# Optimization experiments

Hardware: AMD Instinct MI355X
Metric: run time of the kernel (lower is better)

## Reference

```python
import jax, jax.numpy as jnp
import numpy as np

PILLAR_GROUPS = [[0,1,2],[3,4],[5,6],[7,8,9],[10,11],[12,13,14],[15,16],[17,18],[19],[20,21,22],[23,24,25],[26,27,28]]
N_GROUPS = len(PILLAR_GROUPS)      # 12
MAX_G = max(len(g) for g in PILLAR_GROUPS)  # 3
ENC_DIM = 8
EPS = 1e-5

# static padded gather indices + validity mask so all 12 encoders run in one einsum
_idx = np.zeros((N_GROUPS, MAX_G), np.int32)
_msk = np.zeros((N_GROUPS, MAX_G), np.float32)
for _i, _g in enumerate(PILLAR_GROUPS):
    _idx[_i, :len(_g)] = _g
    _msk[_i, :len(_g)] = 1.0
IDX = jnp.asarray(_idx)
MASK = jnp.asarray(_msk)


def bn(h, gamma, beta, mean, var):
    # BatchNorm1d in eval mode (running statistics)
    return gamma * (h - mean) * jax.lax.rsqrt(var + EPS) + beta


def setup_inputs() -> dict:
    key = jax.random.key(0)
    ks = jax.random.split(key, 40)
    B = 524288

    def rn(k, shape, s=0.2):
        return jax.random.normal(k, shape, jnp.float32) * s

    def bn_params(k, d):
        k1, k2, k3, k4 = jax.random.split(k, 4)
        return (1.0 + rn(k1, (d,), 0.05),          # gamma
                rn(k2, (d,), 0.05),                 # beta
                rn(k3, (d,), 0.1),                  # running_mean
                0.5 + jax.random.uniform(k4, (d,), jnp.float32))  # running_var > 0

    g1, bb1, m1, v1 = bn_params(ks[10], 64)
    g2, bb2, m2, v2 = bn_params(ks[11], 32)
    g3, bb3, m3, v3 = bn_params(ks[12], 16)
    eg, ebt, em, ev = bn_params(ks[13], ENC_DIM)
    # per-encoder BN params: [12, 8]
    eg = jnp.tile(eg, (N_GROUPS, 1)) + rn(ks[14], (N_GROUPS, ENC_DIM), 0.02)
    ebt = jnp.tile(ebt, (N_GROUPS, 1)) + rn(ks[15], (N_GROUPS, ENC_DIM), 0.02)
    em = jnp.tile(em, (N_GROUPS, 1)) + rn(ks[16], (N_GROUPS, ENC_DIM), 0.02)
    ev = jnp.tile(ev, (N_GROUPS, 1)) + 0.1 * jax.random.uniform(ks[17], (N_GROUPS, ENC_DIM))

    return {
        "x": jax.random.normal(ks[0], (B, 29), jnp.float32),
        "We": rn(ks[1], (N_GROUPS, MAX_G, ENC_DIM)),  # padded; pad rows hit zeroed x
        "be": rn(ks[2], (N_GROUPS, ENC_DIM)),
        "enc_gamma": eg, "enc_beta": ebt, "enc_mean": em, "enc_var": ev,
        "Wa": rn(ks[3], (ENC_DIM * N_GROUPS, N_GROUPS)),
        "ba": rn(ks[4], (N_GROUPS,)),
        "W1": rn(ks[5], (ENC_DIM * N_GROUPS, 64)), "b1": rn(ks[6], (64,)),
        "g1": g1, "bb1": bb1, "m1": m1, "v1": v1,
        "W2": rn(ks[7], (64, 32)), "b2": rn(ks[8], (32,)),
        "g2": g2, "bb2": bb2, "m2": m2, "v2": v2,
        "W3": rn(ks[9], (32, 16)), "b3": rn(ks[18], (16,)),
        "g3": g3, "bb3": bb3, "m3": m3, "v3": v3,
        "W4": rn(ks[19], (16, 1)), "b4": rn(ks[20], (1,)),
    }


def reference(x, We, be, enc_gamma, enc_beta, enc_mean, enc_var,
              Wa, ba, W1, b1, g1, bb1, m1, v1,
              W2, b2, g2, bb2, m2, v2,
              W3, b3, g3, bb3, m3, v3, W4, b4):
    B = x.shape[0]
    # gather each pillar group (padded to MAX_G, pads zeroed) -> [B, 12, 3]
    xg = x[:, IDX] * MASK
    # all 12 encoders: Linear + ReLU + BN(eval)  -> reps [B, 12, 8]
    reps = jax.nn.relu(jnp.einsum('bgi,gio->bgo', xg, We) + be)
    reps = bn(reps, enc_gamma, enc_beta, enc_mean, enc_var)
    stacked = reps.reshape(B, -1)                      # [B, 96] (cat order matches)
    weights = jax.nn.softmax(stacked @ Wa + ba, axis=1)  # [B, 12]
    attended = (reps * weights[:, :, None]).reshape(B, -1)  # [B, 96]
    h = bn(jax.nn.relu(attended @ W1 + b1), g1, bb1, m1, v1)  # dropout = identity (eval)
    h = bn(jax.nn.relu(h @ W2 + b2), g2, bb2, m2, v2)
    h = bn(jax.nn.relu(h @ W3 + b3), g3, bb3, m3, v3)
    return jax.nn.sigmoid(h @ W4 + b4)[:, 0]           # squeeze(1) -> [B]
```

## Files before the change

### kernel.cpp

```cpp
#include <hip/hip_runtime.h>
#include <math.h>


typedef _Float16 f16x8 __attribute__((ext_vector_type(8)));
typedef float    f32x4 __attribute__((ext_vector_type(4)));

#define EPS 1e-5f

__device__ __forceinline__ float rcp_fast(float v) { return __builtin_amdgcn_rcpf(v); }

__host__ __device__ constexpr unsigned long long packGS() {
    constexpr int gs[12] = {0,3,5,7,10,12,15,17,19,20,23,26};
    unsigned long long v = 0;
    for (int g = 0; g < 12; ++g) v |= (unsigned long long)gs[g] << (5*g);
    return v;
}
__host__ __device__ constexpr unsigned packGL() {
    constexpr int gl[12] = {3,2,2,3,2,3,2,2,1,3,3,3};
    unsigned v = 0;
    for (int g = 0; g < 12; ++g) v |= (unsigned)gl[g] << (2*g);
    return v;
}

__global__ __launch_bounds__(256, 2) void fused_kernel(
    const float* __restrict__ x,
    const float* __restrict__ We,  const float* __restrict__ be,
    const float* __restrict__ eg,  const float* __restrict__ ebt,
    const float* __restrict__ em,  const float* __restrict__ ev,
    const float* __restrict__ Wa,  const float* __restrict__ ba,
    const float* __restrict__ W1,  const float* __restrict__ b1,
    const float* __restrict__ g1,  const float* __restrict__ bb1,
    const float* __restrict__ m1,  const float* __restrict__ v1,
    const float* __restrict__ W2,  const float* __restrict__ b2,
    const float* __restrict__ g2,  const float* __restrict__ bb2,
    const float* __restrict__ m2,  const float* __restrict__ v2,
    const float* __restrict__ W3,  const float* __restrict__ b3,
    const float* __restrict__ g3,  const float* __restrict__ bb3,
    const float* __restrict__ m3,  const float* __restrict__ v3,
    const float* __restrict__ W4,  const float* __restrict__ b4,
    float* __restrict__ out, int B, int ntiles)
{
    __shared__ __align__(16) char smem_raw[32768];
    const int lane = threadIdx.x & 63;
    const int wave = threadIdx.x >> 6;
    const int l15  = lane & 15;
    const int quad = lane >> 4;

    char* sw = smem_raw + wave * 8192;
    _Float16* repT = (_Float16*)(sw);
    float*    wT   = (float*)   (sw + 3328);
    _Float16* h1T  = (_Float16*)(sw + 4416);
    _Float16* h2T  = (_Float16*)(sw + 6720);

    constexpr unsigned long long GS = packGS();
    constexpr unsigned GL = packGL();

    f16x8 Benc[6];
    #pragma unroll
    for (int t = 0; t < 6; ++t) {
        const int n = t*16 + l15;
        const int g = n >> 3, o = n & 7;
        const int gs = (int)((GS >> (5*g)) & 31);
        const int gl = (int)((GL >> (2*g)) & 3);
        #pragma unroll
        for (int j = 0; j < 8; ++j) {
            const int k  = quad*8 + j;
            const int ji = k - gs;
            float v = (ji >= 0 && ji < gl) ? We[(g*3 + ji)*8 + o] : 0.f;
            Benc[t][j] = (_Float16)v;
        }
    }
    f16x8 Bwa[3];
    #pragma unroll
    for (int s = 0; s < 3; ++s) {
        #pragma unroll
        for (int j = 0; j < 8; ++j) {
            const int k = s*32 + quad*8 + j;
            float v = (l15 < 12) ? Wa[k*12 + l15] : 0.f;
            Bwa[s][j] = (_Float16)v;
        }
    }
    f16x8 Bw1[12];
    #pragma unroll
    for (int t = 0; t < 4; ++t)
        #pragma unroll
        for (int s = 0; s < 3; ++s)
            #pragma unroll
            for (int j = 0; j < 8; ++j) {
                const int k = s*32 + quad*8 + j;
                Bw1[t*3 + s][j] = (_Float16)W1[k*64 + t*16 + l15];
            }
    f16x8 Bw2[4];
    #pragma unroll
    for (int t = 0; t < 2; ++t)
        #pragma unroll
        for (int s = 0; s < 2; ++s)
            #pragma unroll
            for (int j = 0; j < 8; ++j) {
                const int k = s*32 + quad*8 + j;
                Bw2[t*2 + s][j] = (_Float16)W2[k*32 + t*16 + l15];
            }
    f16x8 Bw3;
    #pragma unroll
    for (int j = 0; j < 8; ++j)
        Bw3[j] = (_Float16)W3[(quad*8 + j)*16 + l15];

    float encB[6], encS[6], encT[6];
    #pragma unroll
    for (int t = 0; t < 6; ++t) {
        const int c = t*16 + l15;
        float s = eg[c] * rsqrtf(ev[c] + EPS);
        encS[t] = s; encT[t] = ebt[c] - em[c]*s; encB[t] = be[c];
    }
    const float baL = (l15 < 12) ? ba[l15] : -1e4f;
    float b1L[4], s1L[4], t1L[4];
    #pragma unroll
    for (int t = 0; t < 4; ++t) {
        const int c = t*16 + l15;
        float s = g1[c] * rsqrtf(v1[c] + EPS);
        s1L[t] = s; t1L[t] = bb1[c] - m1[c]*s; b1L[t] = b1[c];
    }
    float b2L[2], s2L[2], t2L[2];
    #pragma unroll
    for (int t = 0; t < 2; ++t) {
        const int c = t*16 + l15;
        float s = g2[c] * rsqrtf(v2[c] + EPS);
        s2L[t] = s; t2L[t] = bb2[c] - m2[c]*s; b2L[t] = b2[c];
    }
    const float sv3 = g3[l15] * rsqrtf(v3[l15] + EPS);
    const float b3L = b3[l15], s3L = sv3, t3L = bb3[l15] - m3[l15]*sv3;
    const float w4L = W4[l15];
    const float b4v = b4[0];

    const int tile0 = blockIdx.x * 32;
    int tile1 = tile0 + 32; if (tile1 > ntiles) tile1 = ntiles;

    for (int tile = tile0 + wave; tile < tile1; tile += 4) {
        const int rowbase = tile << 4;

        int xr = rowbase + l15; if (xr > B-1) xr = B-1;
        const float* xp = x + (size_t)xr*29 + quad*8;
        float xv[8];
        if (quad < 3) {
            #pragma unroll
            for (int j = 0; j < 8; ++j) xv[j] = xp[j];
        } else {
            #pragma unroll
            for (int j = 0; j < 5; ++j) xv[j] = xp[j];
            xv[5] = xv[6] = xv[7] = 0.f;
        }
        f16x8 ax;
        #pragma unroll
        for (int j = 0; j < 8; ++j) ax[j] = (_Float16)xv[j];

        #pragma unroll
        for (int t = 0; t < 6; ++t) {
            f32x4 c = { encB[t], encB[t], encB[t], encB[t] };
            c = __builtin_amdgcn_mfma_f32_16x16x32_f16(ax, Benc[t], c, 0, 0, 0);
            #pragma unroll
            for (int r = 0; r < 4; ++r) {
                float v = fmaf(fmaxf(c[r], 0.f), encS[t], encT[t]);
                repT[(quad*4 + r)*104 + t*16 + l15] = (_Float16)v;
            }
        }

        f32x4 c2 = { baL, baL, baL, baL };
        #pragma unroll
        for (int s = 0; s < 3; ++s) {
            f16x8 a = *(const f16x8*)(repT + l15*104 + s*32 + quad*8);
            c2 = __builtin_amdgcn_mfma_f32_16x16x32_f16(a, Bwa[s], c2, 0, 0, 0);
        }
        #pragma unroll
        for (int r = 0; r < 4; ++r) {
            float v = c2[r];
            float mx = v;
            mx = fmaxf(mx, __shfl_xor(mx, 1));
            mx = fmaxf(mx, __shfl_xor(mx, 2));
            mx = fmaxf(mx, __shfl_xor(mx, 4));
            mx = fmaxf(mx, __shfl_xor(mx, 8));
            float e = __expf(v - mx);
            float sm = e;
            sm += __shfl_xor(sm, 1);
            sm += __shfl_xor(sm, 2);
            sm += __shfl_xor(sm, 4);
            sm += __shfl_xor(sm, 8);
            wT[(quad*4 + r)*17 + l15] = e * rcp_fast(sm);
        }

        f32x4 c3[4];
        #pragma unroll
        for (int t = 0; t < 4; ++t) c3[t] = { b1L[t], b1L[t], b1L[t], b1L[t] };
        #pragma unroll
        for (int s = 0; s < 3; ++s) {
            f16x8 a = *(const f16x8*)(repT + l15*104 + s*32 + quad*8);
            _Float16 wh = (_Float16)wT[l15*17 + s*4 + quad];
            f16x8 aw;
            #pragma unroll
            for (int j = 0; j < 8; ++j) aw[j] = a[j] * wh;
            #pragma unroll
            for (int t = 0; t < 4; ++t)
                c3[t] = __builtin_amdgcn_mfma_f32_16x16x32_f16(aw, Bw1[t*3 + s], c3[t], 0, 0, 0);
        }
        #pragma unroll
        for (int t = 0; t < 4; ++t)
            #pragma unroll
            for (int r = 0; r < 4; ++r) {
                float v = fmaf(fmaxf(c3[t][r], 0.f), s1L[t], t1L[t]);
                h1T[(quad*4 + r)*72 + t*16 + l15] = (_Float16)v;
            }

        f32x4 c4[2];
        #pragma unroll
        for (int t = 0; t < 2; ++t) c4[t] = { b2L[t], b2L[t], b2L[t], b2L[t] };
        #pragma unroll
        for (int s = 0; s < 2; ++s) {
            f16x8 a = *(const f16x8*)(h1T + l15*72 + s*32 + quad*8);
            #pragma unroll
            for (int t = 0; t < 2; ++t)
                c4[t] = __builtin_amdgcn_mfma_f32_16x16x32_f16(a, Bw2[t*2 + s], c4[t], 0, 0, 0);
        }
        #pragma unroll
        for (int t = 0; t < 2; ++t)
            #pragma unroll
            for (int r = 0; r < 4; ++r) {
                float v = fmaf(fmaxf(c4[t][r], 0.f), s2L[t], t2L[t]);
                h2T[(quad*4 + r)*40 + t*16 + l15] = (_Float16)v;
            }

        f32x4 c5 = { b3L, b3L, b3L, b3L };
        {
            f16x8 a = *(const f16x8*)(h2T + l15*40 + quad*8);
            c5 = __builtin_amdgcn_mfma_f32_16x16x32_f16(a, Bw3, c5, 0, 0, 0);
        }

        float z[4];
        #pragma unroll
        for (int r = 0; r < 4; ++r) {
            float v = fmaf(fmaxf(c5[r], 0.f), s3L, t3L);
            float p = v * w4L;
            p += __shfl_xor(p, 1);
            p += __shfl_xor(p, 2);
            p += __shfl_xor(p, 4);
            p += __shfl_xor(p, 8);
            z[r] = p;
        }
        float zi = (l15 == 0) ? z[0] : (l15 == 1) ? z[1] : (l15 == 2) ? z[2] : z[3];
        if (l15 < 4) {
            int row = rowbase + quad*4 + l15;
            if (row < B)
                out[row] = rcp_fast(1.f + __expf(-(zi + b4v)));
        }
    }
}

extern "C" void kernel_launch(void* const* d_in, const int* in_sizes, int n_in,
                              void* d_out, int out_size, void* d_ws, size_t ws_size,
                              hipStream_t stream)
{
    const float* x   = (const float*)d_in[0];
    const float* We  = (const float*)d_in[1];
    const float* be  = (const float*)d_in[2];
    const float* eg  = (const float*)d_in[3];
    const float* ebt = (const float*)d_in[4];
    const float* em  = (const float*)d_in[5];
    const float* ev  = (const float*)d_in[6];
    const float* Wa  = (const float*)d_in[7];
    const float* ba  = (const float*)d_in[8];
    const float* W1  = (const float*)d_in[9];
    const float* b1  = (const float*)d_in[10];
    const float* g1  = (const float*)d_in[11];
    const float* bb1 = (const float*)d_in[12];
    const float* m1  = (const float*)d_in[13];
    const float* v1  = (const float*)d_in[14];
    const float* W2  = (const float*)d_in[15];
    const float* b2  = (const float*)d_in[16];
    const float* g2  = (const float*)d_in[17];
    const float* bb2 = (const float*)d_in[18];
    const float* m2  = (const float*)d_in[19];
    const float* v2  = (const float*)d_in[20];
    const float* W3  = (const float*)d_in[21];
    const float* b3  = (const float*)d_in[22];
    const float* g3  = (const float*)d_in[23];
    const float* bb3 = (const float*)d_in[24];
    const float* m3  = (const float*)d_in[25];
    const float* v3  = (const float*)d_in[26];
    const float* W4  = (const float*)d_in[27];
    const float* b4  = (const float*)d_in[28];

    const int B = in_sizes[0] / 29;
    const int ntiles = (B + 15) / 16;
    const int blocks = (ntiles + 31) / 32;

    fused_kernel<<<blocks, 256, 0, stream>>>(
        x, We, be, eg, ebt, em, ev, Wa, ba,
        W1, b1, g1, bb1, m1, v1,
        W2, b2, g2, bb2, m2, v2,
        W3, b3, g3, bb3, m3, v3,
        W4, b4, (float*)d_out, B, ntiles);
}
```

Baseline: 197.4 us.

## Process two tiles per wave with prefetched x loads and DPP row reductions

Each wave now handles two 16-row tiles at a time for ILP, and software-prefetches the next pair's x rows into registers while computing the current pair. Cross-lane shuffles for softmax and the final dot product are replaced by DPP row_ror reductions, and outputs are written as one float4 per quad. LDS grows to hold double per-wave buffers, with h2T aliasing repT. Register and LDS pressure rise, which may reduce occupancy, and the float4 store assumes B is a multiple of 16.

```diff
diff --git a/kernel.cpp b/kernel.cpp
--- a/kernel.cpp
+++ b/kernel.cpp
@@ -8,6 +8,21 @@
 #define EPS 1e-5f
 
 __device__ __forceinline__ float rcp_fast(float v) { return __builtin_amdgcn_rcpf(v); }
+
+template<int N>
+__device__ __forceinline__ float dpp_ror(float v) {
+    return __int_as_float(__builtin_amdgcn_update_dpp(
+        0, __float_as_int(v), 0x120 + N, 0xF, 0xF, true));
+}
+__device__ __forceinline__ float row_sum16(float v) {
+    v += dpp_ror<1>(v); v += dpp_ror<2>(v); v += dpp_ror<4>(v); v += dpp_ror<8>(v);
+    return v;
+}
+__device__ __forceinline__ float row_max16(float v) {
+    v = fmaxf(v, dpp_ror<1>(v)); v = fmaxf(v, dpp_ror<2>(v));
+    v = fmaxf(v, dpp_ror<4>(v)); v = fmaxf(v, dpp_ror<8>(v));
+    return v;
+}
 
 __host__ __device__ constexpr unsigned long long packGS() {
     constexpr int gs[12] = {0,3,5,7,10,12,15,17,19,20,23,26};
@@ -40,17 +55,21 @@
     const float* __restrict__ W4,  const float* __restrict__ b4,
     float* __restrict__ out, int B, int ntiles)
 {
-    __shared__ __align__(16) char smem_raw[32768];
+    __shared__ __align__(16) char smem_raw[53760];
     const int lane = threadIdx.x & 63;
     const int wave = threadIdx.x >> 6;
     const int l15  = lane & 15;
     const int quad = lane >> 4;
 
-    char* sw = smem_raw + wave * 8192;
-    _Float16* repT = (_Float16*)(sw);
-    float*    wT   = (float*)   (sw + 3328);
-    _Float16* h1T  = (_Float16*)(sw + 4416);
-    _Float16* h2T  = (_Float16*)(sw + 6720);
+    _Float16* repT[2]; float* wT[2]; _Float16* h1T[2]; _Float16* h2T[2];
+    #pragma unroll
+    for (int u = 0; u < 2; ++u) {
+        char* sw = smem_raw + wave * 13440 + u * 6720;
+        repT[u] = (_Float16*)sw;
+        wT[u]   = (float*)   (sw + 3328);
+        h1T[u]  = (_Float16*)(sw + 4416);
+        h2T[u]  = (_Float16*)sw;
+    }
 
     constexpr unsigned long long GS = packGS();
     constexpr unsigned GL = packGL();
@@ -72,14 +91,12 @@
     }
     f16x8 Bwa[3];
     #pragma unroll
-    for (int s = 0; s < 3; ++s) {
+    for (int s = 0; s < 3; ++s)
         #pragma unroll
         for (int j = 0; j < 8; ++j) {
             const int k = s*32 + quad*8 + j;
-            float v = (l15 < 12) ? Wa[k*12 + l15] : 0.f;
-            Bwa[s][j] = (_Float16)v;
-        }
-    }
+            Bwa[s][j] = (_Float16)((l15 < 12) ? Wa[k*12 + l15] : 0.f);
+        }
     f16x8 Bw1[12];
     #pragma unroll
     for (int t = 0; t < 4; ++t)
@@ -132,124 +149,144 @@
     const float w4L = W4[l15];
     const float b4v = b4[0];
 
-    const int tile0 = blockIdx.x * 32;
-    int tile1 = tile0 + 32; if (tile1 > ntiles) tile1 = ntiles;
-
-    for (int tile = tile0 + wave; tile < tile1; tile += 4) {
-        const int rowbase = tile << 4;
-
-        int xr = rowbase + l15; if (xr > B-1) xr = B-1;
-        const float* xp = x + (size_t)xr*29 + quad*8;
-        float xv[8];
-        if (quad < 3) {
-            #pragma unroll
-            for (int j = 0; j < 8; ++j) xv[j] = xp[j];
-        } else {
-            #pragma unroll
-            for (int j = 0; j < 5; ++j) xv[j] = xp[j];
-            xv[5] = xv[6] = xv[7] = 0.f;
-        }
-        f16x8 ax;
-        #pragma unroll
-        for (int j = 0; j < 8; ++j) ax[j] = (_Float16)xv[j];
-
-        #pragma unroll
-        for (int t = 0; t < 6; ++t) {
-            f32x4 c = { encB[t], encB[t], encB[t], encB[t] };
-            c = __builtin_amdgcn_mfma_f32_16x16x32_f16(ax, Benc[t], c, 0, 0, 0);
+    const int tbase = blockIdx.x * 32 + wave * 2;
+
+    auto loadx = [&](int pp, float (&xv)[2][8]) {
+        #pragma unroll
+        for (int u = 0; u < 2; ++u) {
+            int tl = tbase + 8*pp + u; if (tl > ntiles-1) tl = ntiles-1;
+            int xr = tl*16 + l15;      if (xr > B-1)      xr = B-1;
+            const float* xp = x + (size_t)xr*29 + quad*8;
+            if (quad < 3) {
+                #pragma unroll
+                for (int j = 0; j < 8; ++j) xv[u][j] = xp[j];
+            } else {
+                #pragma unroll
+                for (int j = 0; j < 5; ++j) xv[u][j] = xp[j];
+                xv[u][5] = xv[u][6] = xv[u][7] = 0.f;
+            }
+        }
+    };
+
+    float xcur[2][8];
+    loadx(0, xcur);
+
+    #pragma unroll 1
+    for (int p = 0; p < 4; ++p) {
+        float xnext[2][8];
+        loadx(p < 3 ? p + 1 : 3, xnext);
+
+        f16x8 ax[2];
+        #pragma unroll
+        for (int u = 0; u < 2; ++u)
+            #pragma unroll
+            for (int j = 0; j < 8; ++j) ax[u][j] = (_Float16)xcur[u][j];
+
+        #pragma unroll
+        for (int u = 0; u < 2; ++u)
+            #pragma unroll
+            for (int t = 0; t < 6; ++t) {
+                f32x4 c = { encB[t], encB[t], encB[t], encB[t] };
+                c = __builtin_amdgcn_mfma_f32_16x16x32_f16(ax[u], Benc[t], c, 0, 0, 0);
+                #pragma unroll
+                for (int r = 0; r < 4; ++r)
+                    repT[u][(quad*4 + r)*104 + t*16 + l15] =
+                        (_Float16)fmaf(fmaxf(c[r], 0.f), encS[t], encT[t]);
+            }
+
+        f16x8 afr[2][3];
+        #pragma unroll
+        for (int u = 0; u < 2; ++u)
+            #pragma unroll
+            for (int s = 0; s < 3; ++s)
+                afr[u][s] = *(const f16x8*)(repT[u] + l15*104 + s*32 + quad*8);
+
+        #pragma unroll
+        for (int u = 0; u < 2; ++u) {
+            f32x4 c2 = { baL, baL, baL, baL };
+            #pragma unroll
+            for (int s = 0; s < 3; ++s)
+                c2 = __builtin_amdgcn_mfma_f32_16x16x32_f16(afr[u][s], Bwa[s], c2, 0, 0, 0);
             #pragma unroll
             for (int r = 0; r < 4; ++r) {
-                float v = fmaf(fmaxf(c[r], 0.f), encS[t], encT[t]);
-                repT[(quad*4 + r)*104 + t*16 + l15] = (_Float16)v;
-            }
-        }
-
-        f32x4 c2 = { baL, baL, baL, baL };
-        #pragma unroll
-        for (int s = 0; s < 3; ++s) {
-            f16x8 a = *(const f16x8*)(repT + l15*104 + s*32 + quad*8);
-            c2 = __builtin_amdgcn_mfma_f32_16x16x32_f16(a, Bwa[s], c2, 0, 0, 0);
-        }
-        #pragma unroll
-        for (int r = 0; r < 4; ++r) {
-            float v = c2[r];
-            float mx = v;
-            mx = fmaxf(mx, __shfl_xor(mx, 1));
-            mx = fmaxf(mx, __shfl_xor(mx, 2));
-            mx = fmaxf(mx, __shfl_xor(mx, 4));
-            mx = fmaxf(mx, __shfl_xor(mx, 8));
-            float e = __expf(v - mx);
-            float sm = e;
-            sm += __shfl_xor(sm, 1);
-            sm += __shfl_xor(sm, 2);
-            sm += __shfl_xor(sm, 4);
-            sm += __shfl_xor(sm, 8);
-            wT[(quad*4 + r)*17 + l15] = e * rcp_fast(sm);
-        }
-
-        f32x4 c3[4];
-        #pragma unroll
-        for (int t = 0; t < 4; ++t) c3[t] = { b1L[t], b1L[t], b1L[t], b1L[t] };
-        #pragma unroll
-        for (int s = 0; s < 3; ++s) {
-            f16x8 a = *(const f16x8*)(repT + l15*104 + s*32 + quad*8);
-            _Float16 wh = (_Float16)wT[l15*17 + s*4 + quad];
-            f16x8 aw;
-            #pragma unroll
-            for (int j = 0; j < 8; ++j) aw[j] = a[j] * wh;
+                float v  = c2[r];
+                float mx = row_max16(v);
+                float e  = __expf(v - mx);
+                float sm = row_sum16(e);
+                wT[u][(quad*4 + r)*17 + l15] = e * rcp_fast(sm);
+            }
+        }
+
+        #pragma unroll
+        for (int u = 0; u < 2; ++u) {
+            f32x4 c3[4];
+            #pragma unroll
+            for (int t = 0; t < 4; ++t) c3[t] = { b1L[t], b1L[t], b1L[t], b1L[t] };
+            #pragma unroll
+            for (int s = 0; s < 3; ++s) {
+                _Float16 wh = (_Float16)wT[u][l15*17 + s*4 + quad];
+                f16x8 aw;
+                #pragma unroll
+                for (int j = 0; j < 8; ++j) aw[j] = afr[u][s][j] * wh;
+                #pragma unroll
+                for (int t = 0; t < 4; ++t)
+                    c3[t] = __builtin_amdgcn_mfma_f32_16x16x32_f16(aw, Bw1[t*3 + s], c3[t], 0, 0, 0);
+            }
             #pragma unroll
             for (int t = 0; t < 4; ++t)
-                c3[t] = __builtin_amdgcn_mfma_f32_16x16x32_f16(aw, Bw1[t*3 + s], c3[t], 0, 0, 0);
-        }
-        #pragma unroll
-        for (int t = 0; t < 4; ++t)
+                #pragma unroll
+                for (int r = 0; r < 4; ++r)
+                    h1T[u][(quad*4 + r)*72 + t*16 + l15] =
+                        (_Float16)fmaf(fmaxf(c3[t][r], 0.f), s1L[t], t1L[t]);
+        }
+
+        #pragma unroll
+        for (int u = 0; u < 2; ++u) {
+            f32x4 c4[2];
+            #pragma unroll
+            for (int t = 0; t < 2; ++t) c4[t] = { b2L[t], b2L[t], b2L[t], b2L[t] };
+            #pragma unroll
+            for (int s = 0; s < 2; ++s) {
+                f16x8 a = *(const f16x8*)(h1T[u] + l15*72 + s*32 + quad*8);
+                #pragma unroll
+                for (int t = 0; t < 2; ++t)
+                    c4[t] = __builtin_amdgcn_mfma_f32_16x16x32_f16(a, Bw2[t*2 + s], c4[t], 0, 0, 0);
+            }
+            #pragma unroll
+            for (int t = 0; t < 2; ++t)
+                #pragma unroll
+                for (int r = 0; r < 4; ++r)
+                    h2T[u][(quad*4 + r)*40 + t*16 + l15] =
+                        (_Float16)fmaf(fmaxf(c4[t][r], 0.f), s2L[t], t2L[t]);
+        }
+
+        #pragma unroll
+        for (int u = 0; u < 2; ++u) {
+            f32x4 c5 = { b3L, b3L, b3L, b3L };
+            f16x8 a = *(const f16x8*)(h2T[u] + l15*40 + quad*8);
+            c5 = __builtin_amdgcn_mfma_f32_16x16x32_f16(a, Bw3, c5, 0, 0, 0);
+
+            float z[4];
             #pragma unroll
             for (int r = 0; r < 4; ++r) {
-                float v = fmaf(fmaxf(c3[t][r], 0.f), s1L[t], t1L[t]);
-                h1T[(quad*4 + r)*72 + t*16 + l15] = (_Float16)v;
-            }
-
-        f32x4 c4[2];
-        #pragma unroll
-        for (int t = 0; t < 2; ++t) c4[t] = { b2L[t], b2L[t], b2L[t], b2L[t] };
-        #pragma unroll
-        for (int s = 0; s < 2; ++s) {
-            f16x8 a = *(const f16x8*)(h1T + l15*72 + s*32 + quad*8);
-            #pragma unroll
-            for (int t = 0; t < 2; ++t)
-                c4[t] = __builtin_amdgcn_mfma_f32_16x16x32_f16(a, Bw2[t*2 + s], c4[t], 0, 0, 0);
-        }
-        #pragma unroll
-        for (int t = 0; t < 2; ++t)
-            #pragma unroll
-            for (int r = 0; r < 4; ++r) {
-                float v = fmaf(fmaxf(c4[t][r], 0.f), s2L[t], t2L[t]);
-                h2T[(quad*4 + r)*40 + t*16 + l15] = (_Float16)v;
-            }
-
-        f32x4 c5 = { b3L, b3L, b3L, b3L };
-        {
-            f16x8 a = *(const f16x8*)(h2T + l15*40 + quad*8);
-            c5 = __builtin_amdgcn_mfma_f32_16x16x32_f16(a, Bw3, c5, 0, 0, 0);
-        }
-
-        float z[4];
-        #pragma unroll
-        for (int r = 0; r < 4; ++r) {
-            float v = fmaf(fmaxf(c5[r], 0.f), s3L, t3L);
-            float p = v * w4L;
-            p += __shfl_xor(p, 1);
-            p += __shfl_xor(p, 2);
-            p += __shfl_xor(p, 4);
-            p += __shfl_xor(p, 8);
-            z[r] = p;
-        }
-        float zi = (l15 == 0) ? z[0] : (l15 == 1) ? z[1] : (l15 == 2) ? z[2] : z[3];
-        if (l15 < 4) {
-            int row = rowbase + quad*4 + l15;
-            if (row < B)
-                out[row] = rcp_fast(1.f + __expf(-(zi + b4v)));
-        }
+                float v = fmaf(fmaxf(c5[r], 0.f), s3L, t3L);
+                z[r] = row_sum16(v * w4L);
+            }
+            const int tl = tbase + 8*p + u;
+            if (l15 == 0 && tl < ntiles) {
+                float4 o;
+                o.x = rcp_fast(1.f + __expf(-(z[0] + b4v)));
+                o.y = rcp_fast(1.f + __expf(-(z[1] + b4v)));
+                o.z = rcp_fast(1.f + __expf(-(z[2] + b4v)));
+                o.w = rcp_fast(1.f + __expf(-(z[3] + b4v)));
+                *(float4*)(out + tl*16 + quad*4) = o;
+            }
+        }
+
+        #pragma unroll
+        for (int u = 0; u < 2; ++u)
+            #pragma unroll
+            for (int j = 0; j < 8; ++j) xcur[u][j] = xnext[u][j];
     }
 }
 
```

New measurement: 235.1 us. +19.1%, slower.
